# Kernel tuning notes

Hardware: AMD Instinct MI355X
Metric: run time of the kernel (lower is better)

Reference implementation:

```python
import jax, jax.numpy as jnp
import numpy as np
from jax import lax

B, CI, CO, H, W = 8, 64, 64, 256, 256
M1 = M2 = 16
RANK, NEXP, SCALING = 4, 15, 0.1
G = 4  # expert_region_size = sqrt(num_experts + 1)
WF = W // 2 + 1

# expert i occupies grid cell (row, col) = ((i+1)//G, (i+1)%G); cell (0,0) is the base weights1 corner
_IDX = np.arange(1, NEXP + 1)
RR = jnp.asarray(_IDX // G)
CC = jnp.asarray(_IDX % G)


def setup_inputs() -> dict:
    key = jax.random.key(0)
    ks = jax.random.split(key, 20)
    rn = lambda k, shape, s: jax.random.normal(k, shape, jnp.float32) * s
    scale = 1.0 / (CI * CO)
    return {
        "x": rn(ks[0], (B, CI, H, W), 1.0),
        "w1_re": jax.random.uniform(ks[1], (CI, CO, M1, M2), jnp.float32) * scale,
        "w1_im": jax.random.uniform(ks[2], (CI, CO, M1, M2), jnp.float32) * scale,
        "w2_re": jax.random.uniform(ks[3], (CI, CO, M1, M2), jnp.float32) * scale,
        "w2_im": jax.random.uniform(ks[4], (CI, CO, M1, M2), jnp.float32) * scale,
        "la1_re": rn(ks[5], (NEXP, RANK, CI), 0.02),
        "la1_im": rn(ks[6], (NEXP, RANK, CI), 0.02),
        "lb1_re": rn(ks[7], (NEXP, CO, RANK, M1, M2), 0.02),
        "lb1_im": rn(ks[8], (NEXP, CO, RANK, M1, M2), 0.02),
        "la2_re": rn(ks[9], (NEXP, RANK, CI), 0.02),
        "la2_im": rn(ks[10], (NEXP, RANK, CI), 0.02),
        "lb2_re": rn(ks[11], (NEXP, CO, RANK, M1, M2), 0.02),
        "lb2_im": rn(ks[12], (NEXP, CO, RANK, M1, M2), 0.02),
        "gate1": rn(ks[13], (NEXP,), 0.1),
        "gate2": rn(ks[14], (NEXP,), 0.1),
    }


def reference(x, w1_re, w1_im, w2_re, w2_im,
              la1_re, la1_im, lb1_re, lb1_im,
              la2_re, la2_im, lb2_re, lb2_im,
              gate1, gate2):
    x_ft = jnp.fft.rfft2(x)  # [B, CI, H, WF] complex64

    # scalar gates (gate_on_data=False): sigmoid(gate / temperature), temperature=1
    g1 = jax.nn.sigmoid(gate1)  # [E]
    g2 = jax.nn.sigmoid(gate2)
    sploss = jnp.mean(g1) + jnp.mean(g2)

    w1 = lax.complex(w1_re, w1_im)
    w2 = lax.complex(w2_re, w2_im)
    la1 = lax.complex(la1_re, la1_im)
    lb1 = lax.complex(lb1_re, lb1_im)
    la2 = lax.complex(la2_re, la2_im)
    lb2 = lax.complex(lb2_re, lb2_im)

    # per-expert LoRA weights: sum_r lora_b[o,r,x,y] * lora_a[r,i] -> [E, I, O, M1, M2]
    lw1 = jnp.einsum("eri,eorxy->eioxy", la1, lb1) * SCALING
    lw2 = jnp.einsum("eri,eorxy->eioxy", la2, lb2) * SCALING

    # base corner products
    top_base = jnp.einsum("bixy,ioxy->boxy", x_ft[:, :, :M1, :M2], w1)
    bot_base = jnp.einsum("bixy,ioxy->boxy", x_ft[:, :, H - M1:, :M2], w2)

    # gather all expert input tiles at once via a GxG grid view of the low-freq corners
    top = x_ft[:, :, :G * M1, :G * M2].reshape(B, CI, G, M1, G, M2)
    topt = jnp.transpose(top, (2, 4, 0, 1, 3, 5))        # [G, G, B, CI, M1, M2]
    xe1 = topt[RR, CC]                                    # [E, B, CI, M1, M2]
    bot = x_ft[:, :, H - G * M1:, :G * M2].reshape(B, CI, G, M1, G, M2)
    bott = jnp.transpose(bot, (2, 4, 0, 1, 3, 5))
    xe2 = bott[G - 1 - RR, CC]  # rows H-row_end:H-row_start == bottom-grid block 3-row_idx

    oe1 = jnp.einsum("ebixy,eioxy->eboxy", xe1, lw1) * g1[:, None, None, None, None]
    oe2 = jnp.einsum("ebixy,eioxy->eboxy", xe2, lw2) * g2[:, None, None, None, None]

    # scatter all disjoint tiles back into out_ft
    out_top = jnp.zeros((G, G, B, CO, M1, M2), jnp.complex64)
    out_top = out_top.at[0, 0].set(top_base).at[RR, CC].set(oe1)
    out_bot = jnp.zeros((G, G, B, CO, M1, M2), jnp.complex64)
    out_bot = out_bot.at[G - 1, 0].set(bot_base).at[G - 1 - RR, CC].set(oe2)

    out_ft = jnp.zeros((B, CO, H, WF), jnp.complex64)
    top_full = jnp.transpose(out_top, (2, 3, 0, 4, 1, 5)).reshape(B, CO, G * M1, G * M2)
    bot_full = jnp.transpose(out_bot, (2, 3, 0, 4, 1, 5)).reshape(B, CO, G * M1, G * M2)
    out_ft = out_ft.at[:, :, :G * M1, :G * M2].set(top_full)
    out_ft = out_ft.at[:, :, H - G * M1:, :G * M2].set(bot_full)

    y = jnp.fft.irfft2(out_ft, s=(H, W))
    return (y, sploss)
```

## Files before the change

kernel.cpp:

```cpp
#include <hip/hip_runtime.h>
#include <math.h>

#define B_   8
#define CI_  64
#define CO_  64
#define H_   256
#define W_   256
#define NE_  15
#define RK_  4

typedef __attribute__((ext_vector_type(8))) short short8;
typedef __attribute__((ext_vector_type(4))) float f32x4;

__device__ __forceinline__ unsigned bf16u(float f) {
  return (__float_as_uint(f) + 0x8000u) >> 16;
}
__device__ __forceinline__ unsigned pk2(float lo, float hi) {
  return ((__float_as_uint(lo) + 0x8000u) >> 16) |
         ((__float_as_uint(hi) + 0x8000u) & 0xFFFF0000u);
}
__device__ __forceinline__ float ubf(unsigned short u) {
  return __uint_as_float(((unsigned)u) << 16);
}
__device__ __forceinline__ void gload16(const void* g, void* l) {
  __builtin_amdgcn_global_load_lds(
      (const __attribute__((address_space(1))) unsigned int*)g,
      (__attribute__((address_space(3))) unsigned int*)l, 16, 0, 0);
}

__global__ __launch_bounds__(256) void kTab(unsigned short* __restrict__ TAt,
                                            unsigned short* __restrict__ TB,
                                            unsigned short* __restrict__ TD,
                                            unsigned short* __restrict__ TEt) {
  int idx = blockIdx.x * 256 + threadIdx.x;
  const float C = 6.28318530717958647692f / 256.f;
  if (idx < 32768) {
    int n = idx >> 8, q = idx & 255;
    int w = n >> 1, pl = n & 1;
    int mm = (q * w) & 255;
    float s, c; sincosf(C * (float)mm, &s, &c);
    TAt[idx] = (unsigned short)bf16u(pl ? -s : c);
    return;
  }
  idx -= 32768;
  if (idx < 131072) {
    int mrow = idx >> 9, k = idx & 511;
    int p = k >> 1, tt = k & 1;
    int hr = mrow & 127, imr = mrow >> 7;
    int h = (hr < 64) ? hr : hr + 128;
    int mm = (p * h) & 255;
    float s, c; sincosf(C * (float)mm, &s, &c);
    float v = (imr == 0) ? (tt == 0 ? c : s) : (tt == 0 ? -s : c);
    TB[idx] = (unsigned short)bf16u(v);
    return;
  }
  idx -= 131072;
  if (idx < 131072) {
    int mrow = idx >> 8, k = idx & 255;
    int hr = k >> 1, tt = k & 1;
    int p = mrow & 255, imr = mrow >> 8;
    int h = (hr < 64) ? hr : hr + 128;
    int mm = (p * h) & 255;
    float s, c; sincosf(C * (float)mm, &s, &c);
    float v = (imr == 0) ? (tt == 0 ? c : -s) : (tt == 0 ? s : c);
    TD[idx] = (unsigned short)bf16u(v);
    return;
  }
  idx -= 131072;
  if (idx < 32768) {
    int q = idx >> 7, k = idx & 127;
    int w = k >> 1, pl = k & 1;
    int mm = (q * w) & 255;
    float s, c; sincosf(C * (float)mm, &s, &c);
    float v = (pl == 0) ? ((w == 0 ? 1.f : 2.f * c) / 65536.f)
                        : ((w == 0 ? 0.f : -2.f * s) / 65536.f);
    TEt[idx] = (unsigned short)bf16u(v);
  }
}

__global__ __launch_bounds__(512, 6) void kAB(const float* __restrict__ x,
                                              const unsigned short* __restrict__ TAt,
                                              const unsigned short* __restrict__ TB,
                                              unsigned short* __restrict__ Xf) {
  __shared__ unsigned short As[8192];
  __shared__ unsigned short XcL[64 * 264];
  int t = threadIdx.x, lane = t & 63, wid = t >> 6;
  int bi = blockIdx.x;
  const float* xb = x + (size_t)bi * 65536;
  int lrow = lane & 15, lk = (lane >> 4) * 8, jhi = lane >> 4;
  f32x4 acc2[2][4];
#pragma unroll
  for (int a = 0; a < 2; ++a)
#pragma unroll
    for (int b = 0; b < 4; ++b) acc2[a][b] = (f32x4){0.f, 0.f, 0.f, 0.f};

  for (int half = 0; half < 2; ++half) {
    f32x4 acc1[2][4];
#pragma unroll
    for (int a = 0; a < 2; ++a)
#pragma unroll
      for (int b = 0; b < 4; ++b) acc1[a][b] = (f32x4){0.f, 0.f, 0.f, 0.f};
    int mb1 = (wid >> 1) * 32, nb1 = (wid & 1) * 64;
    for (int kk = 0; kk < 8; ++kk) {
      int k0 = kk * 32;
      __syncthreads();
      {
        int r = t >> 2, seg = t & 3;
        int ssw = (seg ^ ((r >> 1) & 3)) * 8;
        const float* xp = xb + (size_t)(half * 128 + r) * 256 + k0 + ssw;
        float4 v0 = *(const float4*)(xp);
        float4 v1 = *(const float4*)(xp + 4);
        uint4 o;
        o.x = pk2(v0.x, v0.y); o.y = pk2(v0.z, v0.w);
        o.z = pk2(v1.x, v1.y); o.w = pk2(v1.z, v1.w);
        *(uint4*)&As[r * 32 + seg * 8] = o;
        gload16(&TAt[r * 256 + k0 + ssw], &As[4096 + t * 8]);
      }
      __syncthreads();
      short8 af[2], bf[4];
#pragma unroll
      for (int a = 0; a < 2; ++a) {
        int row = mb1 + a * 16 + lrow;
        af[a] = *(const short8*)&As[row * 32 + ((jhi ^ ((row >> 1) & 3))) * 8];
      }
#pragma unroll
      for (int b = 0; b < 4; ++b) {
        int row = nb1 + b * 16 + lrow;
        bf[b] = *(const short8*)&As[4096 + row * 32 + ((jhi ^ ((row >> 1) & 3))) * 8];
      }
#pragma unroll
      for (int a = 0; a < 2; ++a)
#pragma unroll
        for (int b = 0; b < 4; ++b)
          acc1[a][b] = __builtin_amdgcn_mfma_f32_16x16x32_bf16(af[a], bf[b], acc1[a][b], 0, 0, 0);
    }
    __syncthreads();
#pragma unroll
    for (int a = 0; a < 2; ++a)
#pragma unroll
      for (int b = 0; b < 4; ++b)
#pragma unroll
        for (int r = 0; r < 4; ++r) {
          int m = mb1 + a * 16 + (lane >> 4) * 4 + r;
          int n = nb1 + b * 16 + lrow;
          XcL[(n >> 1) * 264 + 2 * m + (n & 1)] = (unsigned short)bf16u(acc1[a][b][r]);
        }
    __syncthreads();
    int mb2 = wid * 32;
    for (int kk = 0; kk < 8; ++kk) {
      int k0 = kk * 32;
      __syncthreads();
#pragma unroll
      for (int j = 0; j < 2; ++j) {
        int c = j * 512 + t;
        int m = c >> 2, seg = c & 3;
        int ssw = (seg ^ ((m >> 1) & 3)) * 8;
        gload16(&TB[m * 512 + half * 256 + k0 + ssw], &As[c * 8]);
      }
      __syncthreads();
      short8 af2[2], bf2[4];
#pragma unroll
      for (int a = 0; a < 2; ++a) {
        int row = mb2 + a * 16 + lrow;
        af2[a] = *(const short8*)&As[row * 32 + ((jhi ^ ((row >> 1) & 3))) * 8];
      }
#pragma unroll
      for (int b = 0; b < 4; ++b)
        bf2[b] = *(const short8*)&XcL[(b * 16 + lrow) * 264 + k0 + lk];
#pragma unroll
      for (int a = 0; a < 2; ++a)
#pragma unroll
        for (int b = 0; b < 4; ++b)
          acc2[a][b] = __builtin_amdgcn_mfma_f32_16x16x32_bf16(af2[a], bf2[b], acc2[a][b], 0, 0, 0);
    }
  }
  unsigned short* dst = Xf + (size_t)bi * 16384;
#pragma unroll
  for (int a = 0; a < 2; ++a)
#pragma unroll
    for (int b = 0; b < 4; ++b)
#pragma unroll
      for (int r = 0; r < 4; ++r) {
        int m = wid * 32 + a * 16 + (lane >> 4) * 4 + r;
        int n = b * 16 + lrow;
        dst[m * 64 + n] = (unsigned short)bf16u(acc2[a][b][r]);
      }
}

__global__ __launch_bounds__(256) void kT(const unsigned short* __restrict__ Xf,
                                          float2* __restrict__ T,
                                          const float* __restrict__ la1re,
                                          const float* __restrict__ la1im,
                                          const float* __restrict__ la2re,
                                          const float* __restrict__ la2im) {
  int bid = blockIdx.x;
  int b = bid & 7;
  int e = (bid >> 3) % 15;
  int reg = bid / 120;
  int ep1 = e + 1;
  int grr = (reg == 0) ? (ep1 >> 2) : (3 - (ep1 >> 2));
  int gc = ep1 & 3;
  int hr0 = reg * 64 + grr * 16;
  int w0 = gc * 16;
  int t = threadIdx.x;
  int xx = t >> 4, yy = t & 15;
  const unsigned short* xp =
      Xf + (size_t)b * 64 * 16384 + (hr0 + xx) * 64 + (w0 + yy);
  const float* lare = (reg == 0) ? la1re : la2re;
  const float* laim = (reg == 0) ? la1im : la2im;
  float ar0 = 0.f, ai0 = 0.f, ar1 = 0.f, ai1 = 0.f;
  float ar2 = 0.f, ai2 = 0.f, ar3 = 0.f, ai3 = 0.f;
#pragma unroll 8
  for (int i = 0; i < 64; ++i) {
    float xr = ubf(xp[(size_t)i * 16384]);
    float xi = ubf(xp[(size_t)i * 16384 + 8192]);
    float l0r = lare[(e * 4 + 0) * 64 + i], l0i = laim[(e * 4 + 0) * 64 + i];
    float l1r = lare[(e * 4 + 1) * 64 + i], l1i = laim[(e * 4 + 1) * 64 + i];
    float l2r = lare[(e * 4 + 2) * 64 + i], l2i = laim[(e * 4 + 2) * 64 + i];
    float l3r = lare[(e * 4 + 3) * 64 + i], l3i = laim[(e * 4 + 3) * 64 + i];
    ar0 += l0r * xr - l0i * xi; ai0 += l0r * xi + l0i * xr;
    ar1 += l1r * xr - l1i * xi; ai1 += l1r * xi + l1i * xr;
    ar2 += l2r * xr - l2i * xi; ai2 += l2r * xi + l2i * xr;
    ar3 += l3r * xr - l3i * xi; ai3 += l3r * xi + l3i * xr;
  }
  float2* dst = T + ((((size_t)reg * 15 + e) * 8 + b) * 256 + t) * 4;
  dst[0] = make_float2(ar0, ai0);
  dst[1] = make_float2(ar1, ai1);
  dst[2] = make_float2(ar2, ai2);
  dst[3] = make_float2(ar3, ai3);
}

__global__ __launch_bounds__(256) void kDM(const unsigned short* __restrict__ Xf,
                                           const float2* __restrict__ T,
                                           unsigned short* __restrict__ Gt,
                                           const float* __restrict__ w1re,
                                           const float* __restrict__ w1im,
                                           const float* __restrict__ w2re,
                                           const float* __restrict__ w2im,
                                           const float* __restrict__ lb1re,
                                           const float* __restrict__ lb1im,
                                           const float* __restrict__ lb2re,
                                           const float* __restrict__ lb2im,
                                           const float* __restrict__ gate1,
                                           const float* __restrict__ gate2) {
  __shared__ unsigned Xs[32 * 4 * 8 * 8];
  if (blockIdx.x < 256) {
    int bid = blockIdx.x;
    int yc = bid & 1, xc = (bid >> 1) & 3, oc = (bid >> 3) & 15, reg = bid >> 7;
    int hrb = (reg == 0) ? xc * 4 : 112 + xc * 4;
    const float* Wre = (reg == 0) ? w1re : w2re;
    const float* Wim = (reg == 0) ? w1im : w2im;
    int t = threadIdx.x;
    int b = t >> 5, o = (t >> 3) & 3, yy = t & 7;
    int og = oc * 4 + o, yyg = yc * 8 + yy;
    float ar[4] = {0.f, 0.f, 0.f, 0.f}, ai[4] = {0.f, 0.f, 0.f, 0.f};
    for (int ch = 0; ch < 2; ++ch) {
      __syncthreads();
#pragma unroll
      for (int j = 0; j < 4; ++j) {
        int seg = t + j * 256;
        int sb = seg >> 7, sx = (seg >> 5) & 3, si = seg & 31;
        int i = ch * 32 + si;
        const unsigned short* p =
            Xf + (size_t)(sb * 64 + i) * 16384 + (hrb + sx) * 64 + yc * 8;
        uint4 re = *(const uint4*)p;
        uint4 im = *(const uint4*)(p + 8192);
        uint4 o0, o1;
        o0.x = (re.x & 0xFFFFu) | (im.x << 16);
        o0.y = (re.x >> 16) | (im.x & 0xFFFF0000u);
        o0.z = (re.y & 0xFFFFu) | (im.y << 16);
        o0.w = (re.y >> 16) | (im.y & 0xFFFF0000u);
        o1.x = (re.z & 0xFFFFu) | (im.z << 16);
        o1.y = (re.z >> 16) | (im.z & 0xFFFF0000u);
        o1.z = (re.w & 0xFFFFu) | (im.w << 16);
        o1.w = (re.w >> 16) | (im.w & 0xFFFF0000u);
        uint4* d = (uint4*)&Xs[((si * 4 + sx) * 8 + sb) * 8];
        d[0] = o0; d[1] = o1;
      }
      __syncthreads();
      for (int ic = 0; ic < 32; ++ic) {
        int i = ch * 32 + ic;
#pragma unroll
        for (int xs = 0; xs < 4; ++xs) {
          unsigned pk = Xs[((ic * 4 + xs) * 8 + b) * 8 + yy];
          float xr = ubf((unsigned short)(pk & 0xFFFFu));
          float xi = ubf((unsigned short)(pk >> 16));
          int widx = ((i * 64 + og) * 16 + xc * 4 + xs) * 16 + yyg;
          float wr = Wre[widx], wi = Wim[widx];
          ar[xs] += xr * wr - xi * wi;
          ai[xs] += xr * wi + xi * wr;
        }
      }
    }
    uint4 ov;
    ov.x = pk2(ar[0], ai[0]);
    ov.y = pk2(ar[1], ai[1]);
    ov.z = pk2(ar[2], ai[2]);
    ov.w = pk2(ar[3], ai[3]);
    *(uint4*)(Gt + ((size_t)(b * 64 + og) * 64 + yyg) * 256 + 2 * hrb) = ov;
  } else {
    int bid = blockIdx.x - 256;
    int xc = bid & 3, hrc = (bid >> 2) & 7, oc = bid >> 5;
    int t = threadIdx.x;
    int w = t & 63, og = t >> 6;
    int o = oc * 4 + og;
    int reg = hrc >> 2;
    int grr = hrc & 3;
    int gc = w >> 4, yy = w & 15;
    int e = (reg == 0) ? (4 * grr + gc - 1) : (4 * (3 - grr) + gc - 1);
    if (e < 0) return;
    float gate = (reg == 0) ? gate1[e] : gate2[e];
    float g = 0.1f / (1.f + __expf(-gate));
    const float* lbre = (reg == 0) ? lb1re : lb2re;
    const float* lbim = (reg == 0) ? lb1im : lb2im;
    size_t lbb = ((size_t)(e * 64 + o) * 4) * 256 + yy;
    float blr[4][4], bli[4][4];
#pragma unroll
    for (int x2 = 0; x2 < 4; ++x2) {
      int xx = xc * 4 + x2;
      const float* pr = lbre + lbb + xx * 16;
      const float* pi = lbim + lbb + xx * 16;
#pragma unroll
      for (int r = 0; r < 4; ++r) {
        blr[x2][r] = pr[r * 256];
        bli[x2][r] = pi[r * 256];
      }
    }
    const size_t tbase = (((size_t)reg * 15 + e) * 8) * 256 + yy;
    for (int b = 0; b < 8; ++b) {
      const float4* tp = (const float4*)(T + (tbase + (size_t)b * 256) * 4);
      unsigned out4[4];
#pragma unroll
      for (int x2 = 0; x2 < 4; ++x2) {
        int xx = xc * 4 + x2;
        float4 t01 = tp[xx * 32];
        float4 t23 = tp[xx * 32 + 1];
        float ar = 0.f, aim = 0.f;
        ar += t01.x * blr[x2][0] - t01.y * bli[x2][0];
        aim += t01.x * bli[x2][0] + t01.y * blr[x2][0];
        ar += t01.z * blr[x2][1] - t01.w * bli[x2][1];
        aim += t01.z * bli[x2][1] + t01.w * blr[x2][1];
        ar += t23.x * blr[x2][2] - t23.y * bli[x2][2];
        aim += t23.x * bli[x2][2] + t23.y * blr[x2][2];
        ar += t23.z * blr[x2][3] - t23.w * bli[x2][3];
        aim += t23.z * bli[x2][3] + t23.w * blr[x2][3];
        out4[x2] = pk2(g * ar, g * aim);
      }
      *(uint4*)(Gt + ((size_t)(b * 64 + o) * 64 + w) * 256 + hrc * 32 + xc * 8) =
          make_uint4(out4[0], out4[1], out4[2], out4[3]);
    }
  }
}

__global__ __launch_bounds__(512) void kDE(const unsigned short* __restrict__ Gt,
                                           const unsigned short* __restrict__ TD,
                                           const unsigned short* __restrict__ TEt,
                                           float* __restrict__ y) {
  __shared__ __align__(16) char smem[77824];
  unsigned short* As  = (unsigned short*)smem;
  unsigned short* Bs  = (unsigned short*)(smem + 32768);
  unsigned short* ZL  = (unsigned short*)smem;
  unsigned short* Bs2 = (unsigned short*)(smem + 69632);
  int t = threadIdx.x, lane = t & 63, wid = t >> 6;
  int bo = blockIdx.x;
  const unsigned short* Grow = Gt + (size_t)bo * 16384;
  int lrow = lane & 15, lk = (lane >> 4) * 8, jhi = lane >> 4;

  {
    int mb = wid * 64;
    f32x4 acc[4][4];
#pragma unroll
    for (int a = 0; a < 4; ++a)
#pragma unroll
      for (int b = 0; b < 4; ++b) acc[a][b] = (f32x4){0.f, 0.f, 0.f, 0.f};
    for (int kk = 0; kk < 8; ++kk) {
      int k0 = kk * 32;
      __syncthreads();
      if (t < 256) {
        int n = t >> 2, seg = t & 3;
        gload16(&Grow[n * 256 + k0 + ((seg ^ (n & 3))) * 8], &Bs[t * 8]);
      }
#pragma unroll
      for (int j = 0; j < 4; ++j) {
        int c = j * 512 + t;
        int m = c >> 2, seg = c & 3;
        gload16(&TD[m * 256 + k0 + ((seg ^ (m & 3))) * 8], &As[c * 8]);
      }
      __syncthreads();
      short8 af[4], bf[4];
#pragma unroll
      for (int a = 0; a < 4; ++a) {
        int row = mb + a * 16 + lrow;
        af[a] = *(const short8*)&As[row * 32 + ((jhi ^ (row & 3))) * 8];
      }
#pragma unroll
      for (int b = 0; b < 4; ++b) {
        int row = b * 16 + lrow;
        bf[b] = *(const short8*)&Bs[row * 32 + ((jhi ^ (row & 3))) * 8];
      }
#pragma unroll
      for (int a = 0; a < 4; ++a)
#pragma unroll
        for (int b = 0; b < 4; ++b)
          acc[a][b] = __builtin_amdgcn_mfma_f32_16x16x32_bf16(af[a], bf[b], acc[a][b], 0, 0, 0);
    }
    __syncthreads();
#pragma unroll
    for (int a = 0; a < 4; ++a)
#pragma unroll
      for (int b = 0; b < 4; ++b)
#pragma unroll
        for (int r = 0; r < 4; ++r) {
          int m = mb + a * 16 + (lane >> 4) * 4 + r;
          int p = m & 255, pl = m >> 8;
          int n = b * 16 + lrow;
          ZL[p * 136 + 2 * n + pl] = (unsigned short)bf16u(acc[a][b][r]);
        }
    __syncthreads();
  }

  int mb2 = (wid >> 1) * 64, nb2 = (wid & 1) * 64;
  for (int qh = 0; qh < 2; ++qh) {
    f32x4 acc[4][4];
#pragma unroll
    for (int a = 0; a < 4; ++a)
#pragma unroll
      for (int b = 0; b < 4; ++b) acc[a][b] = (f32x4){0.f, 0.f, 0.f, 0.f};
    for (int kk = 0; kk < 4; ++kk) {
      int k0 = kk * 32;
      __syncthreads();
      {
        int n = t >> 2, seg = t & 3;
        gload16(&TEt[(qh * 128 + n) * 128 + k0 + ((seg ^ (n & 3))) * 8], &Bs2[t * 8]);
      }
      __syncthreads();
      short8 af[4], bf[4];
#pragma unroll
      for (int a = 0; a < 4; ++a)
        af[a] = *(const short8*)&ZL[(mb2 + a * 16 + lrow) * 136 + k0 + lk];
#pragma unroll
      for (int b = 0; b < 4; ++b) {
        int row = nb2 + b * 16 + lrow;
        bf[b] = *(const short8*)&Bs2[row * 32 + ((jhi ^ (row & 3))) * 8];
      }
#pragma unroll
      for (int a = 0; a < 4; ++a)
#pragma unroll
        for (int b = 0; b < 4; ++b)
          acc[a][b] = __builtin_amdgcn_mfma_f32_16x16x32_bf16(af[a], bf[b], acc[a][b], 0, 0, 0);
    }
    float* dst = y + (size_t)bo * 65536 + qh * 128;
#pragma unroll
    for (int a = 0; a < 4; ++a)
#pragma unroll
      for (int b = 0; b < 4; ++b)
#pragma unroll
        for (int r = 0; r < 4; ++r) {
          int p = mb2 + a * 16 + (lane >> 4) * 4 + r;
          int q = nb2 + b * 16 + lrow;
          dst[(size_t)p * 256 + q] = acc[a][b][r];
        }
  }
}

__global__ void kS2(const float* __restrict__ gate1, const float* __restrict__ gate2,
                    float* __restrict__ out) {
  if (threadIdx.x == 0) {
    float s = 0.f;
    for (int e = 0; e < NE_; ++e)
      s += 1.f / (1.f + expf(-gate1[e])) + 1.f / (1.f + expf(-gate2[e]));
    out[0] = s / (float)NE_;
  }
}

extern "C" void kernel_launch(void* const* d_in, const int* in_sizes, int n_in,
                              void* d_out, int out_size, void* d_ws, size_t ws_size,
                              hipStream_t stream) {
  const float* x     = (const float*)d_in[0];
  const float* w1re  = (const float*)d_in[1];
  const float* w1im  = (const float*)d_in[2];
  const float* w2re  = (const float*)d_in[3];
  const float* w2im  = (const float*)d_in[4];
  const float* la1re = (const float*)d_in[5];
  const float* la1im = (const float*)d_in[6];
  const float* lb1re = (const float*)d_in[7];
  const float* lb1im = (const float*)d_in[8];
  const float* la2re = (const float*)d_in[9];
  const float* la2im = (const float*)d_in[10];
  const float* lb2re = (const float*)d_in[11];
  const float* lb2im = (const float*)d_in[12];
  const float* gate1 = (const float*)d_in[13];
  const float* gate2 = (const float*)d_in[14];

  char* ws = (char*)d_ws;
  unsigned short* Xf  = (unsigned short*)(ws + ((size_t)32 << 20));
  unsigned short* Gt  = (unsigned short*)(ws + ((size_t)48 << 20));
  unsigned short* TAt = (unsigned short*)(ws + ((size_t)96 << 20));
  unsigned short* TB  = TAt + 32768;
  unsigned short* TD  = TB + 131072;
  unsigned short* TEt = TD + 131072;
  float2* Tw = (float2*)(ws + ((size_t)97 << 20));
  float* y = (float*)d_out;

  kTab<<<1280, 256, 0, stream>>>(TAt, TB, TD, TEt);
  kAB<<<512, 512, 0, stream>>>(x, TAt, TB, Xf);
  kT<<<240, 256, 0, stream>>>(Xf, Tw, la1re, la1im, la2re, la2im);
  kDM<<<768, 256, 0, stream>>>(Xf, Tw, Gt, w1re, w1im, w2re, w2im,
                               lb1re, lb1im, lb2re, lb2im, gate1, gate2);
  kDE<<<512, 512, 0, stream>>>(Gt, TD, TEt, y);
  kS2<<<1, 64, 0, stream>>>(gate1, gate2, y + (size_t)B_ * CO_ * H_ * W_);
}
```

Measured before the change: 406.7 us.

## Double-buffer shared-memory tiles in kAB and kDE GEMM loops with prefetch

Converts the K-loops of the row-DFT/column-DFT GEMM stages in kAB and the first GEMM in kDE to double-buffered shared memory, prefetching the next K-slice with async global-to-LDS loads while the current slice feeds MFMA. Explicit s_waitcnt vmcnt counts and raw s_barrier replace paired __syncthreads to overlap memory latency with compute. It increases LDS use (kAB drops the occupancy hint of 6 and adds a second buffer), which can lower occupancy. The hand-tuned waitcnt values are fragile if the compiler reorders or splits loads.

```diff
diff --git a/kernel.cpp b/kernel.cpp
--- a/kernel.cpp
+++ b/kernel.cpp
@@ -78,16 +78,18 @@
   }
 }
 
-__global__ __launch_bounds__(512, 6) void kAB(const float* __restrict__ x,
-                                              const unsigned short* __restrict__ TAt,
-                                              const unsigned short* __restrict__ TB,
-                                              unsigned short* __restrict__ Xf) {
-  __shared__ unsigned short As[8192];
+__global__ __launch_bounds__(512) void kAB(const float* __restrict__ x,
+                                           const unsigned short* __restrict__ TAt,
+                                           const unsigned short* __restrict__ TB,
+                                           unsigned short* __restrict__ Xf) {
+  __shared__ unsigned short S[2][8192];
   __shared__ unsigned short XcL[64 * 264];
   int t = threadIdx.x, lane = t & 63, wid = t >> 6;
   int bi = blockIdx.x;
   const float* xb = x + (size_t)bi * 65536;
   int lrow = lane & 15, lk = (lane >> 4) * 8, jhi = lane >> 4;
+  int rs = t >> 2, sg = t & 3;
+  int ssw = (sg ^ ((rs >> 1) & 3)) * 8;
   f32x4 acc2[2][4];
 #pragma unroll
   for (int a = 0; a < 2; ++a)
@@ -101,32 +103,46 @@
 #pragma unroll
       for (int b = 0; b < 4; ++b) acc1[a][b] = (f32x4){0.f, 0.f, 0.f, 0.f};
     int mb1 = (wid >> 1) * 32, nb1 = (wid & 1) * 64;
+    const float* xrowp = xb + (size_t)(half * 128 + rs) * 256 + ssw;
+    float4 xv0 = *(const float4*)(xrowp);
+    float4 xv1 = *(const float4*)(xrowp + 4);
+    asm volatile("" ::: "memory");
+    gload16(&TAt[rs * 256 + ssw], &S[0][4096 + t * 8]);
+#pragma unroll
     for (int kk = 0; kk < 8; ++kk) {
-      int k0 = kk * 32;
-      __syncthreads();
+      int cur = kk & 1;
+      __builtin_amdgcn_s_barrier();
+      __builtin_amdgcn_sched_barrier(0);
       {
-        int r = t >> 2, seg = t & 3;
-        int ssw = (seg ^ ((r >> 1) & 3)) * 8;
-        const float* xp = xb + (size_t)(half * 128 + r) * 256 + k0 + ssw;
-        float4 v0 = *(const float4*)(xp);
-        float4 v1 = *(const float4*)(xp + 4);
         uint4 o;
-        o.x = pk2(v0.x, v0.y); o.y = pk2(v0.z, v0.w);
-        o.z = pk2(v1.x, v1.y); o.w = pk2(v1.z, v1.w);
-        *(uint4*)&As[r * 32 + seg * 8] = o;
-        gload16(&TAt[r * 256 + k0 + ssw], &As[4096 + t * 8]);
-      }
-      __syncthreads();
+        o.x = pk2(xv0.x, xv0.y); o.y = pk2(xv0.z, xv0.w);
+        o.z = pk2(xv1.x, xv1.y); o.w = pk2(xv1.z, xv1.w);
+        *(uint4*)&S[cur][rs * 32 + sg * 8] = o;
+      }
+      if (kk < 7) {
+        int k1 = (kk + 1) * 32;
+        xv0 = *(const float4*)(xrowp + k1);
+        xv1 = *(const float4*)(xrowp + k1 + 4);
+        asm volatile("" ::: "memory");
+        gload16(&TAt[rs * 256 + k1 + ssw], &S[cur ^ 1][4096 + t * 8]);
+        asm volatile("s_waitcnt vmcnt(3)" ::: "memory");
+      } else {
+        asm volatile("s_waitcnt vmcnt(0)" ::: "memory");
+      }
+      asm volatile("s_waitcnt lgkmcnt(0)" ::: "memory");
+      __builtin_amdgcn_sched_barrier(0);
+      __builtin_amdgcn_s_barrier();
+      __builtin_amdgcn_sched_barrier(0);
       short8 af[2], bf[4];
 #pragma unroll
       for (int a = 0; a < 2; ++a) {
         int row = mb1 + a * 16 + lrow;
-        af[a] = *(const short8*)&As[row * 32 + ((jhi ^ ((row >> 1) & 3))) * 8];
+        af[a] = *(const short8*)&S[cur][row * 32 + ((jhi ^ ((row >> 1) & 3))) * 8];
       }
 #pragma unroll
       for (int b = 0; b < 4; ++b) {
         int row = nb1 + b * 16 + lrow;
-        bf[b] = *(const short8*)&As[4096 + row * 32 + ((jhi ^ ((row >> 1) & 3))) * 8];
+        bf[b] = *(const short8*)&S[cur][4096 + row * 32 + ((jhi ^ ((row >> 1) & 3))) * 8];
       }
 #pragma unroll
       for (int a = 0; a < 2; ++a)
@@ -147,22 +163,39 @@
         }
     __syncthreads();
     int mb2 = wid * 32;
+#pragma unroll
+    for (int j = 0; j < 2; ++j) {
+      int c = j * 512 + t;
+      int m = c >> 2, s2 = c & 3;
+      gload16(&TB[m * 512 + half * 256 + ((s2 ^ ((m >> 1) & 3))) * 8], &S[0][c * 8]);
+    }
+#pragma unroll
     for (int kk = 0; kk < 8; ++kk) {
+      int cur = kk & 1;
+      __builtin_amdgcn_s_barrier();
+      __builtin_amdgcn_sched_barrier(0);
+      if (kk < 7) {
+        int k1 = (kk + 1) * 32;
+#pragma unroll
+        for (int j = 0; j < 2; ++j) {
+          int c = j * 512 + t;
+          int m = c >> 2, s2 = c & 3;
+          gload16(&TB[m * 512 + half * 256 + k1 + ((s2 ^ ((m >> 1) & 3))) * 8],
+                  &S[cur ^ 1][c * 8]);
+        }
+        asm volatile("s_waitcnt vmcnt(2)" ::: "memory");
+      } else {
+        asm volatile("s_waitcnt vmcnt(0)" ::: "memory");
+      }
+      __builtin_amdgcn_sched_barrier(0);
+      __builtin_amdgcn_s_barrier();
+      __builtin_amdgcn_sched_barrier(0);
       int k0 = kk * 32;
-      __syncthreads();
-#pragma unroll
-      for (int j = 0; j < 2; ++j) {
-        int c = j * 512 + t;
-        int m = c >> 2, seg = c & 3;
-        int ssw = (seg ^ ((m >> 1) & 3)) * 8;
-        gload16(&TB[m * 512 + half * 256 + k0 + ssw], &As[c * 8]);
-      }
-      __syncthreads();
       short8 af2[2], bf2[4];
 #pragma unroll
       for (int a = 0; a < 2; ++a) {
         int row = mb2 + a * 16 + lrow;
-        af2[a] = *(const short8*)&As[row * 32 + ((jhi ^ ((row >> 1) & 3))) * 8];
+        af2[a] = *(const short8*)&S[cur][row * 32 + ((jhi ^ ((row >> 1) & 3))) * 8];
       }
 #pragma unroll
       for (int b = 0; b < 4; ++b)
@@ -356,11 +389,10 @@
                                            const unsigned short* __restrict__ TD,
                                            const unsigned short* __restrict__ TEt,
                                            float* __restrict__ y) {
-  __shared__ __align__(16) char smem[77824];
-  unsigned short* As  = (unsigned short*)smem;
-  unsigned short* Bs  = (unsigned short*)(smem + 32768);
+  __shared__ __align__(16) char smem[81920];
+  unsigned short* Sb  = (unsigned short*)smem;
   unsigned short* ZL  = (unsigned short*)smem;
-  unsigned short* Bs2 = (unsigned short*)(smem + 69632);
+  unsigned short* Bs2 = (unsigned short*)(smem + 73728);
   int t = threadIdx.x, lane = t & 63, wid = t >> 6;
   int bo = blockIdx.x;
   const unsigned short* Grow = Gt + (size_t)bo * 16384;
@@ -373,30 +405,54 @@
     for (int a = 0; a < 4; ++a)
 #pragma unroll
       for (int b = 0; b < 4; ++b) acc[a][b] = (f32x4){0.f, 0.f, 0.f, 0.f};
+#pragma unroll
+    for (int j = 0; j < 4; ++j) {
+      int c = j * 512 + t;
+      int m = c >> 2, s2 = c & 3;
+      gload16(&TD[m * 256 + ((s2 ^ (m & 3))) * 8], &Sb[c * 8]);
+    }
+    if (t < 256) {
+      int n = t >> 2, s2 = t & 3;
+      gload16(&Grow[n * 256 + ((s2 ^ (n & 3))) * 8], &Sb[16384 + t * 8]);
+    }
+#pragma unroll
     for (int kk = 0; kk < 8; ++kk) {
-      int k0 = kk * 32;
-      __syncthreads();
-      if (t < 256) {
-        int n = t >> 2, seg = t & 3;
-        gload16(&Grow[n * 256 + k0 + ((seg ^ (n & 3))) * 8], &Bs[t * 8]);
-      }
-#pragma unroll
-      for (int j = 0; j < 4; ++j) {
-        int c = j * 512 + t;
-        int m = c >> 2, seg = c & 3;
-        gload16(&TD[m * 256 + k0 + ((seg ^ (m & 3))) * 8], &As[c * 8]);
-      }
-      __syncthreads();
+      int cur = kk & 1;
+      unsigned short* Scur = Sb + cur * 18432;
+      unsigned short* Snxt = Sb + (cur ^ 1) * 18432;
+      __builtin_amdgcn_s_barrier();
+      __builtin_amdgcn_sched_barrier(0);
+      if (kk < 7) {
+        int k1 = (kk + 1) * 32;
+#pragma unroll
+        for (int j = 0; j < 4; ++j) {
+          int c = j * 512 + t;
+          int m = c >> 2, s2 = c & 3;
+          gload16(&TD[m * 256 + k1 + ((s2 ^ (m & 3))) * 8], &Snxt[c * 8]);
+        }
+        if (t < 256) {
+          int n = t >> 2, s2 = t & 3;
+          gload16(&Grow[n * 256 + k1 + ((s2 ^ (n & 3))) * 8], &Snxt[16384 + t * 8]);
+          asm volatile("s_waitcnt vmcnt(5)" ::: "memory");
+        } else {
+          asm volatile("s_waitcnt vmcnt(4)" ::: "memory");
+        }
+      } else {
+        asm volatile("s_waitcnt vmcnt(0)" ::: "memory");
+      }
+      __builtin_amdgcn_sched_barrier(0);
+      __builtin_amdgcn_s_barrier();
+      __builtin_amdgcn_sched_barrier(0);
       short8 af[4], bf[4];
 #pragma unroll
       for (int a = 0; a < 4; ++a) {
         int row = mb + a * 16 + lrow;
-        af[a] = *(const short8*)&As[row * 32 + ((jhi ^ (row & 3))) * 8];
+        af[a] = *(const short8*)&Scur[row * 32 + ((jhi ^ (row & 3))) * 8];
       }
 #pragma unroll
       for (int b = 0; b < 4; ++b) {
         int row = b * 16 + lrow;
-        bf[b] = *(const short8*)&Bs[row * 32 + ((jhi ^ (row & 3))) * 8];
+        bf[b] = *(const short8*)&Scur[16384 + row * 32 + ((jhi ^ (row & 3))) * 8];
       }
 #pragma unroll
       for (int a = 0; a < 4; ++a)
@@ -430,8 +486,8 @@
       int k0 = kk * 32;
       __syncthreads();
       {
-        int n = t >> 2, seg = t & 3;
-        gload16(&TEt[(qh * 128 + n) * 128 + k0 + ((seg ^ (n & 3))) * 8], &Bs2[t * 8]);
+        int n = t >> 2, s2 = t & 3;
+        gload16(&TEt[(qh * 128 + n) * 128 + k0 + ((s2 ^ (n & 3))) * 8], &Bs2[t * 8]);
       }
       __syncthreads();
       short8 af[4], bf[4];
```

After: 379.8 us. 6.6% less time.
